# Kernel tuning notes

Hardware: AMD Instinct MI355X
Metric: run time of the kernel (lower is better)

The kernel has to match this reference:

```python
import jax, jax.numpy as jnp
import numpy as np


def setup_inputs() -> dict:
    key = jax.random.key(0)
    kq, kk, kv = jax.random.split(key, 3)
    B, S, H, D = 2, 2048, 16, 128
    query = jax.random.normal(kq, (B, S, H, D), dtype=jnp.float32)
    k = jax.random.normal(kk, (B, S, H, D), dtype=jnp.float32)
    v = jax.random.normal(kv, (B, S, H, D), dtype=jnp.float32)
    mask = jnp.ones((B, 1, S, S), dtype=jnp.bool_)  # broadcast over heads
    return {"query": query, "key": k, "value": v, "mask": mask}


def reference(query, key, value, mask):
    dtype = query.dtype
    attn_dim = query.shape[-1]
    scale = attn_dim ** (-0.5)
    q = query.astype(jnp.float32) * scale
    k = key.astype(jnp.float32)
    v = value.astype(jnp.float32)
    # scores: [B, H, Q, K] in f32
    qk = jnp.einsum('...qhd,...khd->...hqk', q, k)
    qk = jnp.where(mask, qk, jnp.finfo(jnp.float32).min)
    p = jax.nn.softmax(qk, axis=-1).astype(dtype)
    out = jnp.einsum('...hqk,...khd->...qhd', p, v)
    return out.astype(dtype)
```

## Files before the change

### kernel.cpp

```cpp
#include <hip/hip_runtime.h>

typedef _Float16 f16;
typedef __attribute__((ext_vector_type(4))) float float4_t;
typedef __attribute__((ext_vector_type(8))) _Float16 f16x8;
typedef __attribute__((ext_vector_type(4))) _Float16 f16x4;
typedef __attribute__((ext_vector_type(16))) float f32x16;

#define NB 2
#define NS 2048
#define NH 16
#define ND 128
#define QBLK 128
#define KVB 32
#define NT (NS / KVB)
#define SCALE2 (0.08838834764831845f * 1.4426950408889634f)
#define DEFER_THR 7.2f

__device__ __forceinline__ int vg(int d) { return ((((d >> 1) ^ (d >> 4)) & 3) << 3); }

__global__ __launch_bounds__(256, 2) void fattn_kernel(
    const float* __restrict__ Qg, const float* __restrict__ Kg,
    const float* __restrict__ Vg, float* __restrict__ Og)
{
    __shared__ __align__(16) f16 Ks[2][KVB * ND];
    __shared__ __align__(16) f16 Vts[2][ND * KVB];
    __shared__ __align__(16) f16 Ph[4][32 * 40];

    const int tid  = threadIdx.x;
    const int w    = tid >> 6;
    const int lane = tid & 63;
    const int lq   = lane & 31;
    const int hi   = lane >> 5;

    int wg = (blockIdx.x & 7) * 64 + (blockIdx.x >> 3);
    const int bh = wg >> 4;
    const int qt = wg & 15;
    const int b  = bh >> 4;
    const int h  = bh & 15;
    const int myq = qt * QBLK + w * 32 + lq;

    f16x8 qh[8], ql[8];
    {
        const float* qp = Qg + (((size_t)(b * NS + myq) * NH + h) * ND);
#pragma unroll
        for (int kb = 0; kb < 8; ++kb) {
            const float4_t x0 = *(const float4_t*)(qp + kb * 16 + hi * 8);
            const float4_t x1 = *(const float4_t*)(qp + kb * 16 + hi * 8 + 4);
            const float xv[8] = {x0[0], x0[1], x0[2], x0[3], x1[0], x1[1], x1[2], x1[3]};
#pragma unroll
            for (int i = 0; i < 8; ++i) {
                const float v = xv[i] * SCALE2;
                const f16 vh2 = (f16)v;
                qh[kb][i] = vh2;
                ql[kb][i] = (f16)(v - (float)vh2);
            }
        }
    }

    f32x16 acc[4];
#pragma unroll
    for (int nt = 0; nt < 4; ++nt)
#pragma unroll
        for (int i = 0; i < 16; ++i) acc[nt][i] = 0.0f;

    float mrun = -1e30f, lrun = 0.0f;

    f16* myPh = Ph[w];

    const int sr = tid >> 3;
    const int sc = (tid & 7) * 16;

    float4_t kr[4], vr[4];

    auto LOADT = [&](int kt) {
        const size_t off = (((size_t)(b * NS + kt * KVB + sr) * NH + h) * ND) + sc;
#pragma unroll
        for (int i = 0; i < 4; ++i) kr[i] = *(const float4_t*)(Kg + off + 4 * i);
#pragma unroll
        for (int i = 0; i < 4; ++i) vr[i] = *(const float4_t*)(Vg + off + 4 * i);
    };
    auto STORET = [&](int buf) {
        f16x8 kh0, kh1;
#pragma unroll
        for (int i = 0; i < 4; ++i) {
            kh0[i] = (f16)kr[0][i]; kh0[4 + i] = (f16)kr[1][i];
            kh1[i] = (f16)kr[2][i]; kh1[4 + i] = (f16)kr[3][i];
        }
        const int swk = (sr & 15) * 8;
        *(f16x8*)&Ks[buf][sr * 128 + (sc ^ swk)]       = kh0;
        *(f16x8*)&Ks[buf][sr * 128 + ((sc + 8) ^ swk)] = kh1;
#pragma unroll
        for (int j = 0; j < 16; ++j) {
            const int d = sc + j;
            Vts[buf][d * 32 + (sr ^ vg(d))] = (f16)vr[j >> 2][j & 3];
        }
    };

    int vroff[2][4];
#pragma unroll
    for (int ks = 0; ks < 2; ++ks)
#pragma unroll
        for (int nt = 0; nt < 4; ++nt) {
            const int d = nt * 32 + lq;
            vroff[ks][nt] = d * 32 + ((ks * 16 + hi * 8) ^ vg(d));
        }

    LOADT(0);
    STORET(0);
    LOADT(1);
    __syncthreads();

    int cur = 0;
    for (int kt = 0; kt < NT; ++kt) {
        f32x16 sacc;
#pragma unroll
        for (int i = 0; i < 16; ++i) sacc[i] = 0.0f;
        {
            const f16* ksrow = &Ks[cur][lq * 128];
            __builtin_amdgcn_s_setprio(1);
#pragma unroll
            for (int kb = 0; kb < 8; ++kb) {
                const int c = kb * 16 + hi * 8;
                const f16x8 kf = *(const f16x8*)&ksrow[c ^ ((lq & 15) * 8)];
                sacc = __builtin_amdgcn_mfma_f32_32x32x16_f16(kf, qh[kb], sacc, 0, 0, 0);
                sacc = __builtin_amdgcn_mfma_f32_32x32x16_f16(kf, ql[kb], sacc, 0, 0, 0);
            }
            __builtin_amdgcn_s_setprio(0);
        }

        float sm = sacc[0];
#pragma unroll
        for (int r = 1; r < 16; ++r) sm = fmaxf(sm, sacc[r]);
        sm = fmaxf(sm, __shfl_xor(sm, 32));
        if (!__all(sm - mrun <= DEFER_THR)) {
            const float mnew  = fmaxf(mrun, sm);
            const float alpha = __builtin_amdgcn_exp2f(mrun - mnew);
            lrun *= alpha;
#pragma unroll
            for (int nt = 0; nt < 4; ++nt)
#pragma unroll
                for (int r = 0; r < 16; ++r) acc[nt][r] *= alpha;
            mrun = mnew;
        }
        float rs = 0.0f;
#pragma unroll
        for (int r = 0; r < 16; ++r) {
            sacc[r] = __builtin_amdgcn_exp2f(sacc[r] - mrun);
            rs += sacc[r];
        }
        rs += __shfl_xor(rs, 32);
        lrun += rs;

#pragma unroll
        for (int g = 0; g < 4; ++g) {
            f16x4 p4h;
#pragma unroll
            for (int i = 0; i < 4; ++i) p4h[i] = (f16)sacc[g * 4 + i];
            *(f16x4*)&myPh[lq * 40 + 8 * g + 4 * hi] = p4h;
        }

        {
            const f16* vbuf = Vts[cur];
#pragma unroll
            for (int ks = 0; ks < 2; ++ks) {
                const f16x8 pfh = *(const f16x8*)&myPh[lq * 40 + ks * 16 + hi * 8];
                __builtin_amdgcn_s_setprio(1);
#pragma unroll
                for (int nt = 0; nt < 4; ++nt) {
                    const f16x8 vf = *(const f16x8*)&vbuf[vroff[ks][nt]];
                    acc[nt] = __builtin_amdgcn_mfma_f32_32x32x16_f16(vf, pfh, acc[nt], 0, 0, 0);
                }
                __builtin_amdgcn_s_setprio(0);
            }
        }

        if (kt + 1 < NT) {
            STORET(cur ^ 1);
            if (kt + 2 < NT) LOADT(kt + 2);
            __syncthreads();
        }
        cur ^= 1;
    }

    const float inv = 1.0f / lrun;
    float* op = Og + (((size_t)(b * NS + myq) * NH + h) * ND);
#pragma unroll
    for (int nt = 0; nt < 4; ++nt) {
#pragma unroll
        for (int g = 0; g < 4; ++g) {
            float4_t o4;
#pragma unroll
            for (int i = 0; i < 4; ++i) o4[i] = acc[nt][g * 4 + i] * inv;
            const int d = nt * 32 + 8 * g + 4 * hi;
            *(float4_t*)(op + d) = o4;
        }
    }
}

extern "C" void kernel_launch(void* const* d_in, const int* in_sizes, int n_in,
                              void* d_out, int out_size, void* d_ws, size_t ws_size,
                              hipStream_t stream) {
    const float* Q = (const float*)d_in[0];
    const float* K = (const float*)d_in[1];
    const float* V = (const float*)d_in[2];
    float* O = (float*)d_out;
    dim3 grid(NB * NH * (NS / QBLK));
    dim3 block(256);
    fattn_kernel<<<grid, block, 0, stream>>>(Q, K, V, O);
}
```

Before: 248.9 us.

## Split KV range across two wave groups, drop Q low-part MFMA, shuffle P in registers

Doubles the block to 512 threads, with two groups of four waves each handling half of the KV sequence for the same query tile. The partial outputs and the per-row max and sum are merged through shared memory at the end. It also drops the split-precision low half of Q, which halves the QK MFMAs at some cost in accuracy. The P matrix is now repacked with cvt_pkrtz and a lane shuffle rather than a round trip through LDS. The extra merge step and 512-thread blocks may reduce how many waves can run per CU.

```diff
diff --git a/kernel.cpp b/kernel.cpp
--- a/kernel.cpp
+++ b/kernel.cpp
@@ -1,9 +1,11 @@
 #include <hip/hip_runtime.h>
 
 typedef _Float16 f16;
+typedef __fp16 __attribute__((ext_vector_type(2))) fp16x2;
+typedef __attribute__((ext_vector_type(8))) _Float16 f16x8;
 typedef __attribute__((ext_vector_type(4))) float float4_t;
-typedef __attribute__((ext_vector_type(8))) _Float16 f16x8;
-typedef __attribute__((ext_vector_type(4))) _Float16 f16x4;
+typedef __attribute__((ext_vector_type(2))) float float2_t;
+typedef __attribute__((ext_vector_type(4))) unsigned int u32x4;
 typedef __attribute__((ext_vector_type(16))) float f32x16;
 
 #define NB 2
@@ -12,22 +14,23 @@
 #define ND 128
 #define QBLK 128
 #define KVB 32
-#define NT (NS / KVB)
+#define NTH 32
 #define SCALE2 (0.08838834764831845f * 1.4426950408889634f)
 #define DEFER_THR 7.2f
 
 __device__ __forceinline__ int vg(int d) { return ((((d >> 1) ^ (d >> 4)) & 3) << 3); }
 
-__global__ __launch_bounds__(256, 2) void fattn_kernel(
+__global__ __launch_bounds__(512, 4) void fattn_kernel(
     const float* __restrict__ Qg, const float* __restrict__ Kg,
     const float* __restrict__ Vg, float* __restrict__ Og)
 {
-    __shared__ __align__(16) f16 Ks[2][KVB * ND];
-    __shared__ __align__(16) f16 Vts[2][ND * KVB];
-    __shared__ __align__(16) f16 Ph[4][32 * 40];
+    __shared__ __align__(16) f16 SMEM[32768];
+    __shared__ __align__(16) float2_t Ml[QBLK];
 
     const int tid  = threadIdx.x;
     const int w    = tid >> 6;
+    const int grp  = w >> 2;
+    const int w4   = w & 3;
     const int lane = tid & 63;
     const int lq   = lane & 31;
     const int hi   = lane >> 5;
@@ -37,22 +40,22 @@
     const int qt = wg & 15;
     const int b  = bh >> 4;
     const int h  = bh & 15;
-    const int myq = qt * QBLK + w * 32 + lq;
-
-    f16x8 qh[8], ql[8];
+    const int myq = qt * QBLK + w4 * 32 + lq;
+
+    f16* const Kb = SMEM + grp * 16384;
+    f16* const Vb = SMEM + grp * 16384 + 8192;
+
+    f16x8 qh[8];
     {
         const float* qp = Qg + (((size_t)(b * NS + myq) * NH + h) * ND);
 #pragma unroll
         for (int kb = 0; kb < 8; ++kb) {
             const float4_t x0 = *(const float4_t*)(qp + kb * 16 + hi * 8);
             const float4_t x1 = *(const float4_t*)(qp + kb * 16 + hi * 8 + 4);
-            const float xv[8] = {x0[0], x0[1], x0[2], x0[3], x1[0], x1[1], x1[2], x1[3]};
-#pragma unroll
-            for (int i = 0; i < 8; ++i) {
-                const float v = xv[i] * SCALE2;
-                const f16 vh2 = (f16)v;
-                qh[kb][i] = vh2;
-                ql[kb][i] = (f16)(v - (float)vh2);
+#pragma unroll
+            for (int i = 0; i < 4; ++i) {
+                qh[kb][i]     = (f16)(x0[i] * SCALE2);
+                qh[kb][4 + i] = (f16)(x1[i] * SCALE2);
             }
         }
     }
@@ -65,15 +68,15 @@
 
     float mrun = -1e30f, lrun = 0.0f;
 
-    f16* myPh = Ph[w];
-
-    const int sr = tid >> 3;
-    const int sc = (tid & 7) * 16;
+    const int tg  = tid & 255;
+    const int sr  = tg >> 3;
+    const int sc  = (tg & 7) * 16;
+    const int kv0 = grp * (NS / 2);
 
     float4_t kr[4], vr[4];
 
     auto LOADT = [&](int kt) {
-        const size_t off = (((size_t)(b * NS + kt * KVB + sr) * NH + h) * ND) + sc;
+        const size_t off = (((size_t)(b * NS + kv0 + kt * KVB + sr) * NH + h) * ND) + sc;
 #pragma unroll
         for (int i = 0; i < 4; ++i) kr[i] = *(const float4_t*)(Kg + off + 4 * i);
 #pragma unroll
@@ -87,12 +90,12 @@
             kh1[i] = (f16)kr[2][i]; kh1[4 + i] = (f16)kr[3][i];
         }
         const int swk = (sr & 15) * 8;
-        *(f16x8*)&Ks[buf][sr * 128 + (sc ^ swk)]       = kh0;
-        *(f16x8*)&Ks[buf][sr * 128 + ((sc + 8) ^ swk)] = kh1;
+        *(f16x8*)&Kb[buf * 4096 + sr * 128 + (sc ^ swk)]       = kh0;
+        *(f16x8*)&Kb[buf * 4096 + sr * 128 + ((sc + 8) ^ swk)] = kh1;
 #pragma unroll
         for (int j = 0; j < 16; ++j) {
             const int d = sc + j;
-            Vts[buf][d * 32 + (sr ^ vg(d))] = (f16)vr[j >> 2][j & 3];
+            Vb[buf * 4096 + d * 32 + (sr ^ vg(d))] = (f16)vr[j >> 2][j & 3];
         }
     };
 
@@ -111,19 +114,17 @@
     __syncthreads();
 
     int cur = 0;
-    for (int kt = 0; kt < NT; ++kt) {
+    for (int kt = 0; kt < NTH; ++kt) {
         f32x16 sacc;
 #pragma unroll
         for (int i = 0; i < 16; ++i) sacc[i] = 0.0f;
         {
-            const f16* ksrow = &Ks[cur][lq * 128];
+            const f16* ksrow = Kb + cur * 4096 + lq * 128;
             __builtin_amdgcn_s_setprio(1);
 #pragma unroll
             for (int kb = 0; kb < 8; ++kb) {
-                const int c = kb * 16 + hi * 8;
-                const f16x8 kf = *(const f16x8*)&ksrow[c ^ ((lq & 15) * 8)];
+                const f16x8 kf = *(const f16x8*)&ksrow[(kb * 16 + hi * 8) ^ ((lq & 15) * 8)];
                 sacc = __builtin_amdgcn_mfma_f32_32x32x16_f16(kf, qh[kb], sacc, 0, 0, 0);
-                sacc = __builtin_amdgcn_mfma_f32_32x32x16_f16(kf, ql[kb], sacc, 0, 0, 0);
             }
             __builtin_amdgcn_s_setprio(0);
         }
@@ -151,49 +152,86 @@
         rs += __shfl_xor(rs, 32);
         lrun += rs;
 
-#pragma unroll
-        for (int g = 0; g < 4; ++g) {
-            f16x4 p4h;
-#pragma unroll
-            for (int i = 0; i < 4; ++i) p4h[i] = (f16)sacc[g * 4 + i];
-            *(f16x4*)&myPh[lq * 40 + 8 * g + 4 * hi] = p4h;
-        }
-
+        f16x8 pf[2];
         {
-            const f16* vbuf = Vts[cur];
-#pragma unroll
-            for (int ks = 0; ks < 2; ++ks) {
-                const f16x8 pfh = *(const f16x8*)&myPh[lq * 40 + ks * 16 + hi * 8];
-                __builtin_amdgcn_s_setprio(1);
+            unsigned u[8], x[8];
+#pragma unroll
+            for (int j = 0; j < 8; ++j) {
+                const fp16x2 pk2 = __builtin_amdgcn_cvt_pkrtz(sacc[2 * j], sacc[2 * j + 1]);
+                u[j] = __builtin_bit_cast(unsigned, pk2);
+            }
+#pragma unroll
+            for (int j = 0; j < 8; ++j) x[j] = (unsigned)__shfl_xor((int)u[j], 32);
+            u32x4 a, c;
+            a[0] = hi ? x[2] : u[0];
+            a[1] = hi ? x[3] : u[1];
+            a[2] = hi ? u[2] : x[0];
+            a[3] = hi ? u[3] : x[1];
+            c[0] = hi ? x[6] : u[4];
+            c[1] = hi ? x[7] : u[5];
+            c[2] = hi ? u[6] : x[4];
+            c[3] = hi ? u[7] : x[5];
+            pf[0] = __builtin_bit_cast(f16x8, a);
+            pf[1] = __builtin_bit_cast(f16x8, c);
+        }
+
+        {
+            const f16* vbuf = Vb + cur * 4096;
+            __builtin_amdgcn_s_setprio(1);
+#pragma unroll
+            for (int ks = 0; ks < 2; ++ks)
 #pragma unroll
                 for (int nt = 0; nt < 4; ++nt) {
                     const f16x8 vf = *(const f16x8*)&vbuf[vroff[ks][nt]];
-                    acc[nt] = __builtin_amdgcn_mfma_f32_32x32x16_f16(vf, pfh, acc[nt], 0, 0, 0);
+                    acc[nt] = __builtin_amdgcn_mfma_f32_32x32x16_f16(vf, pf[ks], acc[nt], 0, 0, 0);
                 }
-                __builtin_amdgcn_s_setprio(0);
-            }
-        }
-
-        if (kt + 1 < NT) {
+            __builtin_amdgcn_s_setprio(0);
+        }
+
+        if (kt + 1 < NTH) {
             STORET(cur ^ 1);
-            if (kt + 2 < NT) LOADT(kt + 2);
+            if (kt + 2 < NTH) LOADT(kt + 2);
             __syncthreads();
         }
         cur ^= 1;
     }
 
-    const float inv = 1.0f / lrun;
-    float* op = Og + (((size_t)(b * NS + myq) * NH + h) * ND);
-#pragma unroll
-    for (int nt = 0; nt < 4; ++nt) {
-#pragma unroll
-        for (int g = 0; g < 4; ++g) {
-            float4_t o4;
-#pragma unroll
-            for (int i = 0; i < 4; ++i) o4[i] = acc[nt][g * 4 + i] * inv;
-            const int d = nt * 32 + 8 * g + 4 * hi;
-            *(float4_t*)(op + d) = o4;
-        }
+    __syncthreads();
+    float* const Of = (float*)SMEM;
+    if (grp == 1) {
+#pragma unroll
+        for (int nt = 0; nt < 4; ++nt)
+#pragma unroll
+            for (int r4 = 0; r4 < 4; ++r4) {
+                float4_t t;
+#pragma unroll
+                for (int i = 0; i < 4; ++i) t[i] = acc[nt][r4 * 4 + i];
+                *(float4_t*)&Of[((((w4 * 4 + nt) * 4 + r4) * 64) + lane) * 4] = t;
+            }
+        if (hi == 0) {
+            float2_t ml; ml[0] = mrun; ml[1] = lrun;
+            Ml[w4 * 32 + lq] = ml;
+        }
+    }
+    __syncthreads();
+    if (grp == 0) {
+        const float2_t ml1 = Ml[w4 * 32 + lq];
+        const float ms  = fmaxf(mrun, ml1[0]);
+        const float a0  = __builtin_amdgcn_exp2f(mrun   - ms);
+        const float a1  = __builtin_amdgcn_exp2f(ml1[0] - ms);
+        const float inv = 1.0f / (a0 * lrun + a1 * ml1[1]);
+        float* op = Og + (((size_t)(b * NS + myq) * NH + h) * ND);
+#pragma unroll
+        for (int nt = 0; nt < 4; ++nt)
+#pragma unroll
+            for (int r4 = 0; r4 < 4; ++r4) {
+                const float4_t o1 = *(const float4_t*)&Of[((((w4 * 4 + nt) * 4 + r4) * 64) + lane) * 4];
+                float4_t o;
+#pragma unroll
+                for (int i = 0; i < 4; ++i)
+                    o[i] = (a0 * acc[nt][r4 * 4 + i] + a1 * o1[i]) * inv;
+                *(float4_t*)(op + nt * 32 + 8 * r4 + 4 * hi) = o;
+            }
     }
 }
 
@@ -205,6 +243,6 @@
     const float* V = (const float*)d_in[2];
     float* O = (float*)d_out;
     dim3 grid(NB * NH * (NS / QBLK));
-    dim3 block(256);
+    dim3 block(512);
     fattn_kernel<<<grid, block, 0, stream>>>(Q, K, V, O);
 }
```

Result: slower. 567.3 us (+127.9%).
